# Kernel tuning notes

Measured on AMD Instinct MI355X. Metric: run time of the kernel, lower is better.

Reference implementation:

```python
import jax, jax.numpy as jnp
import numpy as np

# 8 directional difference stencils (N, S, E, W, NE, SE, SW, NW), OIHW [8,1,3,3]
_WINDOWS = np.array([
    [[0, 1, 0], [0, -1, 0], [0, 0, 0]],
    [[0, 0, 0], [0, -1, 0], [0, 1, 0]],
    [[0, 0, 0], [0, -1, 1], [0, 0, 0]],
    [[0, 0, 0], [1, -1, 0], [0, 0, 0]],
    [[0, 0, 1], [0, -1, 0], [0, 0, 0]],
    [[0, 0, 0], [0, -1, 0], [0, 0, 1]],
    [[0, 0, 0], [0, -1, 0], [1, 0, 0]],
    [[1, 0, 0], [0, -1, 0], [0, 0, 0]],
], dtype=np.float32).reshape(8, 1, 3, 3)

ITERATIONS = 30  # int(self.iterations.item()) with init value 30.0


def setup_inputs() -> dict:
    key = jax.random.key(0)
    k1, k2, k3 = jax.random.split(key, 3)
    x = jax.random.normal(k1, (32, 3, 512, 512), dtype=jnp.float32)
    W_expand = jax.random.normal(k2, (3, 3, 1, 1), dtype=jnp.float32) * 0.3
    b_expand = jax.random.normal(k3, (3,), dtype=jnp.float32) * 0.1
    return {
        "x": x,
        "delta": jnp.float32(0.1),
        "kappa": jnp.float32(15.0),
        "W_expand": W_expand,
        "b_expand": b_expand,
    }


def reference(x, delta, kappa, W_expand, b_expand):
    K = jnp.asarray(_WINDOWS)  # [8,1,3,3]
    # axial directions weight 1, diagonal directions weight 1/(sqrt(2))^2 = 0.5
    dir_w = jnp.array([1.0, 1.0, 1.0, 1.0, 0.5, 0.5, 0.5, 0.5],
                      dtype=x.dtype).reshape(1, 8, 1, 1)

    # RGB -> luminance, [B,1,H,W]
    u = (0.299 * x[:, 0] + 0.587 * x[:, 1] + 0.114 * x[:, 2])[:, None]

    def step(u, _):
        # all 8 directional gradients in one grouped conv: [B,8,H,W]
        nabla = jax.lax.conv_general_dilated(
            u, K, window_strides=(1, 1), padding='SAME',
            dimension_numbers=('NCHW', 'OIHW', 'NCHW'))
        diff = 1.0 / (1.0 + (nabla / kappa) ** 2)  # Perona-Malik diffusivity
        upd = jnp.sum(dir_w * diff * nabla, axis=1, keepdims=True)
        return u + delta * upd, None

    u, _ = jax.lax.scan(step, u, None, length=ITERATIONS)

    # repeat to 3 channels then 1x1 conv (expand_channels)
    u_rgb = jnp.repeat(u, 3, axis=1)  # [B,3,H,W]
    out = jnp.einsum('oi,bihw->bohw', W_expand[:, :, 0, 0], u_rgb)
    out = out + b_expand[None, :, None, None]
    return out
```

## Files before the change

kernel.cpp:

```cpp
#include <hip/hip_runtime.h>

#define BATCH 32
#define HGT 512
#define WID 512
#define PLANE (HGT * WID)
#define NPIX (BATCH * PLANE)
#define BSTRIDE (3 * PLANE)
#define WQ (WID / 4)
#define NQUAD (NPIX / 4)

#define RSLAB 16
#define SLABS (HGT / RSLAB)
#define LROWS (RSLAB + 4)
#define BROWS (RSLAB + 2)
#define FBLOCKS (BATCH * SLABS)
#define FTHREADS 512
#define LDS_BYTES ((LROWS + BROWS) * WID * 4)

__device__ __forceinline__ float4 ld4(const float* p) {
    return *reinterpret_cast<const float4*>(p);
}
__device__ __forceinline__ void st4(float* p, float4 v) {
    *reinterpret_cast<float4*>(p) = v;
}

__device__ __forceinline__ float pm_flux(float d, float ik2) {
    return d * __builtin_amdgcn_rcpf(fmaf(d * d, ik2, 1.f));
}

__device__ __forceinline__ void lds_row6(const float* __restrict__ buf, int row, int quad,
                                         float r[6]) {
    const float* p = buf + row * WID + (quad << 2);
    float4 v = ld4(p);
    r[1] = v.x; r[2] = v.y; r[3] = v.z; r[4] = v.w;
    r[0] = (quad > 0) ? p[-1] : 0.f;
    r[5] = (quad < WQ - 1) ? p[4] : 0.f;
}

__device__ __forceinline__ void level_flux(const float a[6], const float b[6],
                                           float vF[4], float seF[5], float swF[5],
                                           float ik2) {
#pragma unroll
    for (int j = 0; j < 4; ++j) vF[j] = pm_flux(b[j + 1] - a[j + 1], ik2);
#pragma unroll
    for (int i = 0; i < 5; ++i) seF[i] = pm_flux(b[i + 1] - a[i], ik2);
#pragma unroll
    for (int i = 0; i < 5; ++i) swF[i] = pm_flux(b[i] - a[i + 1], ik2);
}

template <typename Emit>
__device__ __forceinline__ void strip_from_lds(const float* __restrict__ buf, int L0, int n,
                                               int quad, float delta, float ik2,
                                               Emit&& emit) {
    float a[6], m[6], d6[6];
    lds_row6(buf, L0 - 1, quad, a);
    lds_row6(buf, L0, quad, m);
    float pV[4], pSE[5], pSW[5];
    level_flux(a, m, pV, pSE, pSW, ik2);

    for (int i = 0; i < n; ++i) {
        lds_row6(buf, L0 + i + 1, quad, d6);
        float hF[5];
#pragma unroll
        for (int t = 0; t < 5; ++t) hF[t] = pm_flux(m[t + 1] - m[t], ik2);
        float cV[4], cSE[5], cSW[5];
        level_flux(m, d6, cV, cSE, cSW, ik2);
        float o[4];
#pragma unroll
        for (int j = 0; j < 4; ++j) {
            float axial = cV[j] - pV[j] + hF[j + 1] - hF[j];
            float diag  = cSE[j + 1] + cSW[j] - pSE[j] - pSW[j + 1];
            o[j] = fmaf(delta, fmaf(0.5f, diag, axial), m[j + 1]);
        }
        emit(L0 + i, make_float4(o[0], o[1], o[2], o[3]));
#pragma unroll
        for (int t = 0; t < 6; ++t) m[t] = d6[t];
#pragma unroll
        for (int j = 0; j < 4; ++j) pV[j] = cV[j];
#pragma unroll
        for (int t = 0; t < 5; ++t) { pSE[t] = cSE[t]; pSW[t] = cSW[t]; }
    }
}

template <int MODE>
__global__ __launch_bounds__(FTHREADS, 4)
void pm_fused2(const float* __restrict__ src, int sstr,
               float* __restrict__ dst, int dstr,
               const float* __restrict__ pdelta, const float* __restrict__ pkappa,
               const float* __restrict__ Wexp, const float* __restrict__ bexp) {
    extern __shared__ float lds[];
    float* bufA = lds;
    float* bufB = lds + LROWS * WID;

    const int img  = blockIdx.x >> 5;
    const int slab = blockIdx.x & (SLABS - 1);
    const int H0   = slab * RSLAB;
    const int tid  = threadIdx.x;

    const float delta = *pdelta;
    const float kappa = *pkappa;
    const float ik2 = __builtin_amdgcn_rcpf(kappa * kappa);

    const float* sb = src + (size_t)img * sstr;
#pragma unroll
    for (int i = tid; i < LROWS * WQ; i += FTHREADS) {
        int row  = i >> 7;
        int quad = i & (WQ - 1);
        int g = H0 - 2 + row;
        float4 v = make_float4(0.f, 0.f, 0.f, 0.f);
        if ((unsigned)g < (unsigned)HGT) {
            const float* p = sb + g * WID + (quad << 2);
            if (MODE == 0) {
                float4 r = ld4(p), gg = ld4(p + PLANE), bb = ld4(p + 2 * PLANE);
                v.x = fmaf(0.299f, r.x, fmaf(0.587f, gg.x, 0.114f * bb.x));
                v.y = fmaf(0.299f, r.y, fmaf(0.587f, gg.y, 0.114f * bb.y));
                v.z = fmaf(0.299f, r.z, fmaf(0.587f, gg.z, 0.114f * bb.z));
                v.w = fmaf(0.299f, r.w, fmaf(0.587f, gg.w, 0.114f * bb.w));
            } else {
                v = ld4(p);
            }
        }
        st4(bufA + row * WID + (quad << 2), v);
    }
    __syncthreads();

    const int strip = tid >> 7;
    const int quad  = tid & (WQ - 1);

    {
        int L0 = 1 + 5 * strip - (strip == 3 ? 1 : 0);
        int n  = (strip < 2) ? 5 : 4;
        strip_from_lds(bufA, L0, n, quad, delta, ik2, [&](int L, float4 o) {
            int g = H0 - 2 + L;
            if ((unsigned)g >= (unsigned)HGT) o = make_float4(0.f, 0.f, 0.f, 0.f);
            st4(bufB + (L - 1) * WID + (quad << 2), o);
        });
    }
    __syncthreads();

    float s0 = 0.f, s1 = 0.f, s2 = 0.f, b0 = 0.f, b1 = 0.f, b2 = 0.f;
    if (MODE == 2) {
        s0 = Wexp[0] + Wexp[1] + Wexp[2];
        s1 = Wexp[3] + Wexp[4] + Wexp[5];
        s2 = Wexp[6] + Wexp[7] + Wexp[8];
        b0 = bexp[0]; b1 = bexp[1]; b2 = bexp[2];
    }
    {
        int LB0 = 1 + 4 * strip;
        float* db = dst + (size_t)img * dstr;
        strip_from_lds(bufB, LB0, 4, quad, delta, ik2, [&](int LB, float4 o) {
            int g = H0 - 1 + LB;
            float* p = db + g * WID + (quad << 2);
            if (MODE == 2) {
                st4(p, make_float4(fmaf(s0, o.x, b0), fmaf(s0, o.y, b0),
                                   fmaf(s0, o.z, b0), fmaf(s0, o.w, b0)));
                st4(p + PLANE, make_float4(fmaf(s1, o.x, b1), fmaf(s1, o.y, b1),
                                           fmaf(s1, o.z, b1), fmaf(s1, o.w, b1)));
                st4(p + 2 * PLANE, make_float4(fmaf(s2, o.x, b2), fmaf(s2, o.y, b2),
                                               fmaf(s2, o.z, b2), fmaf(s2, o.w, b2)));
            } else {
                st4(p, o);
            }
        });
    }
}

__global__ void expand_own_v4(float* __restrict__ out,
                              const float* __restrict__ Wexp,
                              const float* __restrict__ bexp) {
    int idx = blockIdx.x * blockDim.x + threadIdx.x;
    if (idx >= NQUAD) return;
    int b = idx / (PLANE / 4);
    int off = (idx - b * (PLANE / 4)) * 4;
    size_t base = (size_t)b * BSTRIDE + off;

    float4 u = ld4(out + base);
    float s0 = Wexp[0] + Wexp[1] + Wexp[2];
    float s1 = Wexp[3] + Wexp[4] + Wexp[5];
    float s2 = Wexp[6] + Wexp[7] + Wexp[8];
    float b0 = bexp[0], b1 = bexp[1], b2 = bexp[2];

    st4(out + base, make_float4(s0 * u.x + b0, s0 * u.y + b0, s0 * u.z + b0, s0 * u.w + b0));
    st4(out + base + PLANE,
        make_float4(s1 * u.x + b1, s1 * u.y + b1, s1 * u.z + b1, s1 * u.w + b1));
    st4(out + base + 2 * PLANE,
        make_float4(s2 * u.x + b2, s2 * u.y + b2, s2 * u.z + b2, s2 * u.w + b2));
}

extern "C" void kernel_launch(void* const* d_in, const int* in_sizes, int n_in,
                              void* d_out, int out_size, void* d_ws, size_t ws_size,
                              hipStream_t stream) {
    const float* x      = (const float*)d_in[0];
    const float* pdelta = (const float*)d_in[1];
    const float* pkappa = (const float*)d_in[2];
    const float* Wexp   = (const float*)d_in[3];
    const float* bexp   = (const float*)d_in[4];
    float* out = (float*)d_out;

    const size_t need = (size_t)2 * NPIX * sizeof(float);
    if (ws_size >= need) {
        float* uA = (float*)d_ws;
        float* uB = uA + NPIX;
        pm_fused2<0><<<FBLOCKS, FTHREADS, LDS_BYTES, stream>>>(
            x, BSTRIDE, uA, PLANE, pdelta, pkappa, Wexp, bexp);
        float* s = uA;
        float* d = uB;
        for (int k = 0; k < 13; ++k) {
            pm_fused2<1><<<FBLOCKS, FTHREADS, LDS_BYTES, stream>>>(
                s, PLANE, d, PLANE, pdelta, pkappa, Wexp, bexp);
            float* t = s; s = d; d = t;
        }
        pm_fused2<2><<<FBLOCKS, FTHREADS, LDS_BYTES, stream>>>(
            s, PLANE, out, BSTRIDE, pdelta, pkappa, Wexp, bexp);
    } else {
        float* uA = out;
        float* uB = out + PLANE;
        pm_fused2<0><<<FBLOCKS, FTHREADS, LDS_BYTES, stream>>>(
            x, BSTRIDE, uA, BSTRIDE, pdelta, pkappa, Wexp, bexp);
        float* s = uA;
        float* d = uB;
        for (int k = 0; k < 14; ++k) {
            pm_fused2<1><<<FBLOCKS, FTHREADS, LDS_BYTES, stream>>>(
                s, BSTRIDE, d, BSTRIDE, pdelta, pkappa, Wexp, bexp);
            float* t = s; s = d; d = t;
        }
        const int block = 256;
        const int grid_q = (NQUAD + block - 1) / block;
        expand_own_v4<<<grid_q, block, 0, stream>>>(out, Wexp, bexp);
    }
}
```

Baseline: 388.7 us.

## Generalize temporal blocking to S fused diffusion steps per launch with single LDS buffer

Templates the fused kernel on the number of time steps S done in LDS per launch, using one in-place buffer with register staging and barriers in place of two ping-pong buffers. The default path now runs 7 launches of 4 steps plus one launch of 2, where it previously ran 15 launches of 2 steps. This cuts global memory round-trips and launch count. In exchange, each launch recomputes wider halos (8 extra rows per 16-row slab), uses more LDS, and adds barriers between steps.

```diff
diff --git a/kernel.cpp b/kernel.cpp
--- a/kernel.cpp
+++ b/kernel.cpp
@@ -11,11 +11,8 @@
 
 #define RSLAB 16
 #define SLABS (HGT / RSLAB)
-#define LROWS (RSLAB + 4)
-#define BROWS (RSLAB + 2)
 #define FBLOCKS (BATCH * SLABS)
-#define FTHREADS 512
-#define LDS_BYTES ((LROWS + BROWS) * WID * 4)
+#define FT 512
 
 __device__ __forceinline__ float4 ld4(const float* p) {
     return *reinterpret_cast<const float4*>(p);
@@ -48,54 +45,28 @@
     for (int i = 0; i < 5; ++i) swF[i] = pm_flux(b[i] - a[i + 1], ik2);
 }
 
-template <typename Emit>
-__device__ __forceinline__ void strip_from_lds(const float* __restrict__ buf, int L0, int n,
-                                               int quad, float delta, float ik2,
-                                               Emit&& emit) {
-    float a[6], m[6], d6[6];
-    lds_row6(buf, L0 - 1, quad, a);
-    lds_row6(buf, L0, quad, m);
-    float pV[4], pSE[5], pSW[5];
-    level_flux(a, m, pV, pSE, pSW, ik2);
-
-    for (int i = 0; i < n; ++i) {
-        lds_row6(buf, L0 + i + 1, quad, d6);
-        float hF[5];
-#pragma unroll
-        for (int t = 0; t < 5; ++t) hF[t] = pm_flux(m[t + 1] - m[t], ik2);
-        float cV[4], cSE[5], cSW[5];
-        level_flux(m, d6, cV, cSE, cSW, ik2);
-        float o[4];
-#pragma unroll
-        for (int j = 0; j < 4; ++j) {
-            float axial = cV[j] - pV[j] + hF[j + 1] - hF[j];
-            float diag  = cSE[j + 1] + cSW[j] - pSE[j] - pSW[j + 1];
-            o[j] = fmaf(delta, fmaf(0.5f, diag, axial), m[j + 1]);
-        }
-        emit(L0 + i, make_float4(o[0], o[1], o[2], o[3]));
-#pragma unroll
-        for (int t = 0; t < 6; ++t) m[t] = d6[t];
-#pragma unroll
-        for (int j = 0; j < 4; ++j) pV[j] = cV[j];
-#pragma unroll
-        for (int t = 0; t < 5; ++t) { pSE[t] = cSE[t]; pSW[t] = cSW[t]; }
-    }
-}
-
-template <int MODE>
-__global__ __launch_bounds__(FTHREADS, 4)
-void pm_fused2(const float* __restrict__ src, int sstr,
+__device__ __forceinline__ void srange(int L0, int L1, int strip, int& s0, int& n) {
+    int tot = L1 - L0;
+    int base = tot >> 2, rem = tot & 3;
+    n = base + (strip < rem ? 1 : 0);
+    s0 = L0 + strip * base + (strip < rem ? strip : rem);
+}
+
+template <int MODE, int S>
+__global__ __launch_bounds__(FT, 4)
+void pm_fusedk(const float* __restrict__ src, int sstr,
                float* __restrict__ dst, int dstr,
                const float* __restrict__ pdelta, const float* __restrict__ pkappa,
                const float* __restrict__ Wexp, const float* __restrict__ bexp) {
-    extern __shared__ float lds[];
-    float* bufA = lds;
-    float* bufB = lds + LROWS * WID;
-
-    const int img  = blockIdx.x >> 5;
-    const int slab = blockIdx.x & (SLABS - 1);
-    const int H0   = slab * RSLAB;
-    const int tid  = threadIdx.x;
+    constexpr int LR = RSLAB + 2 * S;
+    extern __shared__ float buf[];
+
+    const int img   = blockIdx.x >> 5;
+    const int slab  = blockIdx.x & (SLABS - 1);
+    const int H0    = slab * RSLAB;
+    const int tid   = threadIdx.x;
+    const int strip = tid >> 7;
+    const int quad  = tid & (WQ - 1);
 
     const float delta = *pdelta;
     const float kappa = *pkappa;
@@ -103,13 +74,13 @@
 
     const float* sb = src + (size_t)img * sstr;
 #pragma unroll
-    for (int i = tid; i < LROWS * WQ; i += FTHREADS) {
-        int row  = i >> 7;
-        int quad = i & (WQ - 1);
-        int g = H0 - 2 + row;
+    for (int i = tid; i < LR * WQ; i += FT) {
+        int row = i >> 7;
+        int q   = i & (WQ - 1);
+        int g = H0 - S + row;
         float4 v = make_float4(0.f, 0.f, 0.f, 0.f);
         if ((unsigned)g < (unsigned)HGT) {
-            const float* p = sb + g * WID + (quad << 2);
+            const float* p = sb + g * WID + (q << 2);
             if (MODE == 0) {
                 float4 r = ld4(p), gg = ld4(p + PLANE), bb = ld4(p + 2 * PLANE);
                 v.x = fmaf(0.299f, r.x, fmaf(0.587f, gg.x, 0.114f * bb.x));
@@ -120,71 +91,115 @@
                 v = ld4(p);
             }
         }
-        st4(bufA + row * WID + (quad << 2), v);
+        st4(buf + row * WID + (q << 2), v);
     }
     __syncthreads();
 
-    const int strip = tid >> 7;
-    const int quad  = tid & (WQ - 1);
-
-    {
-        int L0 = 1 + 5 * strip - (strip == 3 ? 1 : 0);
-        int n  = (strip < 2) ? 5 : 4;
-        strip_from_lds(bufA, L0, n, quad, delta, ik2, [&](int L, float4 o) {
-            int g = H0 - 2 + L;
-            if ((unsigned)g >= (unsigned)HGT) o = make_float4(0.f, 0.f, 0.f, 0.f);
-            st4(bufB + (L - 1) * WID + (quad << 2), o);
-        });
-    }
-    __syncthreads();
-
-    float s0 = 0.f, s1 = 0.f, s2 = 0.f, b0 = 0.f, b1 = 0.f, b2 = 0.f;
+    float s0c = 0.f, s1c = 0.f, s2c = 0.f, b0c = 0.f, b1c = 0.f, b2c = 0.f;
     if (MODE == 2) {
-        s0 = Wexp[0] + Wexp[1] + Wexp[2];
-        s1 = Wexp[3] + Wexp[4] + Wexp[5];
-        s2 = Wexp[6] + Wexp[7] + Wexp[8];
-        b0 = bexp[0]; b1 = bexp[1]; b2 = bexp[2];
-    }
-    {
-        int LB0 = 1 + 4 * strip;
-        float* db = dst + (size_t)img * dstr;
-        strip_from_lds(bufB, LB0, 4, quad, delta, ik2, [&](int LB, float4 o) {
-            int g = H0 - 1 + LB;
-            float* p = db + g * WID + (quad << 2);
-            if (MODE == 2) {
-                st4(p, make_float4(fmaf(s0, o.x, b0), fmaf(s0, o.y, b0),
-                                   fmaf(s0, o.z, b0), fmaf(s0, o.w, b0)));
-                st4(p + PLANE, make_float4(fmaf(s1, o.x, b1), fmaf(s1, o.y, b1),
-                                           fmaf(s1, o.z, b1), fmaf(s1, o.w, b1)));
-                st4(p + 2 * PLANE, make_float4(fmaf(s2, o.x, b2), fmaf(s2, o.y, b2),
-                                               fmaf(s2, o.z, b2), fmaf(s2, o.w, b2)));
-            } else {
-                st4(p, o);
+        s0c = Wexp[0] + Wexp[1] + Wexp[2];
+        s1c = Wexp[3] + Wexp[4] + Wexp[5];
+        s2c = Wexp[6] + Wexp[7] + Wexp[8];
+        b0c = bexp[0]; b1c = bexp[1]; b2c = bexp[2];
+    }
+
+    float* db = dst + (size_t)img * dstr;
+
+#pragma unroll
+    for (int s = 0; s < S; ++s) {
+        const int L0r = s + 1, L1r = LR - 1 - s;
+        int st0, n;
+        srange(L0r, L1r, strip, st0, n);
+
+        float4 res[6];
+        float a[6], m[6], d6[6];
+        lds_row6(buf, st0 - 1, quad, a);
+        lds_row6(buf, st0, quad, m);
+        float pV[4], pSE[5], pSW[5];
+        level_flux(a, m, pV, pSE, pSW, ik2);
+
+#pragma unroll
+        for (int i = 0; i < 6; ++i) {
+            if (i < n) {
+                lds_row6(buf, st0 + i + 1, quad, d6);
+                float hF[5];
+#pragma unroll
+                for (int t = 0; t < 5; ++t) hF[t] = pm_flux(m[t + 1] - m[t], ik2);
+                float cV[4], cSE[5], cSW[5];
+                level_flux(m, d6, cV, cSE, cSW, ik2);
+                float o[4];
+#pragma unroll
+                for (int j = 0; j < 4; ++j) {
+                    float axial = cV[j] - pV[j] + hF[j + 1] - hF[j];
+                    float diag  = cSE[j + 1] + cSW[j] - pSE[j] - pSW[j + 1];
+                    o[j] = fmaf(delta, fmaf(0.5f, diag, axial), m[j + 1]);
+                }
+                int g = H0 - S + st0 + i;
+                bool in = (unsigned)g < (unsigned)HGT;
+                res[i] = in ? make_float4(o[0], o[1], o[2], o[3])
+                            : make_float4(0.f, 0.f, 0.f, 0.f);
+#pragma unroll
+                for (int t = 0; t < 6; ++t) m[t] = d6[t];
+#pragma unroll
+                for (int j = 0; j < 4; ++j) pV[j] = cV[j];
+#pragma unroll
+                for (int t = 0; t < 5; ++t) { pSE[t] = cSE[t]; pSW[t] = cSW[t]; }
             }
-        });
-    }
-}
-
-__global__ void expand_own_v4(float* __restrict__ out,
-                              const float* __restrict__ Wexp,
-                              const float* __restrict__ bexp) {
+        }
+
+        if (s == S - 1) {
+#pragma unroll
+            for (int i = 0; i < 6; ++i) {
+                if (i < n) {
+                    int g = H0 - S + st0 + i;
+                    float* p = db + g * WID + (quad << 2);
+                    if (MODE == 2) {
+                        float4 u = res[i];
+                        st4(p, make_float4(fmaf(s0c, u.x, b0c), fmaf(s0c, u.y, b0c),
+                                           fmaf(s0c, u.z, b0c), fmaf(s0c, u.w, b0c)));
+                        st4(p + PLANE,
+                            make_float4(fmaf(s1c, u.x, b1c), fmaf(s1c, u.y, b1c),
+                                        fmaf(s1c, u.z, b1c), fmaf(s1c, u.w, b1c)));
+                        st4(p + 2 * PLANE,
+                            make_float4(fmaf(s2c, u.x, b2c), fmaf(s2c, u.y, b2c),
+                                        fmaf(s2c, u.z, b2c), fmaf(s2c, u.w, b2c)));
+                    } else {
+                        st4(p, res[i]);
+                    }
+                }
+            }
+        } else {
+            __syncthreads();
+#pragma unroll
+            for (int i = 0; i < 6; ++i)
+                if (i < n) st4(buf + (st0 + i) * WID + (quad << 2), res[i]);
+            __syncthreads();
+        }
+    }
+}
+
+__global__ void expand_from(const float* __restrict__ usrc, int ustr,
+                            float* __restrict__ out,
+                            const float* __restrict__ Wexp,
+                            const float* __restrict__ bexp) {
     int idx = blockIdx.x * blockDim.x + threadIdx.x;
     if (idx >= NQUAD) return;
     int b = idx / (PLANE / 4);
     int off = (idx - b * (PLANE / 4)) * 4;
-    size_t base = (size_t)b * BSTRIDE + off;
-
-    float4 u = ld4(out + base);
+
+    float4 u = ld4(usrc + (size_t)b * ustr + off);
     float s0 = Wexp[0] + Wexp[1] + Wexp[2];
     float s1 = Wexp[3] + Wexp[4] + Wexp[5];
     float s2 = Wexp[6] + Wexp[7] + Wexp[8];
     float b0 = bexp[0], b1 = bexp[1], b2 = bexp[2];
 
-    st4(out + base, make_float4(s0 * u.x + b0, s0 * u.y + b0, s0 * u.z + b0, s0 * u.w + b0));
-    st4(out + base + PLANE,
-        make_float4(s1 * u.x + b1, s1 * u.y + b1, s1 * u.z + b1, s1 * u.w + b1));
-    st4(out + base + 2 * PLANE,
-        make_float4(s2 * u.x + b2, s2 * u.y + b2, s2 * u.z + b2, s2 * u.w + b2));
+    size_t base = (size_t)b * BSTRIDE + off;
+    st4(out + base, make_float4(fmaf(s0, u.x, b0), fmaf(s0, u.y, b0),
+                                fmaf(s0, u.z, b0), fmaf(s0, u.w, b0)));
+    st4(out + base + PLANE, make_float4(fmaf(s1, u.x, b1), fmaf(s1, u.y, b1),
+                                        fmaf(s1, u.z, b1), fmaf(s1, u.w, b1)));
+    st4(out + base + 2 * PLANE, make_float4(fmaf(s2, u.x, b2), fmaf(s2, u.y, b2),
+                                            fmaf(s2, u.z, b2), fmaf(s2, u.w, b2)));
 }
 
 extern "C" void kernel_launch(void* const* d_in, const int* in_sizes, int n_in,
@@ -197,35 +212,40 @@
     const float* bexp   = (const float*)d_in[4];
     float* out = (float*)d_out;
 
+    const int LDS4 = (RSLAB + 8) * WID * 4;
+    const int LDS2 = (RSLAB + 4) * WID * 4;
+
     const size_t need = (size_t)2 * NPIX * sizeof(float);
     if (ws_size >= need) {
         float* uA = (float*)d_ws;
         float* uB = uA + NPIX;
-        pm_fused2<0><<<FBLOCKS, FTHREADS, LDS_BYTES, stream>>>(
+        pm_fusedk<0, 4><<<FBLOCKS, FT, LDS4, stream>>>(
             x, BSTRIDE, uA, PLANE, pdelta, pkappa, Wexp, bexp);
         float* s = uA;
         float* d = uB;
-        for (int k = 0; k < 13; ++k) {
-            pm_fused2<1><<<FBLOCKS, FTHREADS, LDS_BYTES, stream>>>(
+        for (int k = 0; k < 6; ++k) {
+            pm_fusedk<1, 4><<<FBLOCKS, FT, LDS4, stream>>>(
                 s, PLANE, d, PLANE, pdelta, pkappa, Wexp, bexp);
             float* t = s; s = d; d = t;
         }
-        pm_fused2<2><<<FBLOCKS, FTHREADS, LDS_BYTES, stream>>>(
+        pm_fusedk<2, 2><<<FBLOCKS, FT, LDS2, stream>>>(
             s, PLANE, out, BSTRIDE, pdelta, pkappa, Wexp, bexp);
     } else {
         float* uA = out;
         float* uB = out + PLANE;
-        pm_fused2<0><<<FBLOCKS, FTHREADS, LDS_BYTES, stream>>>(
+        pm_fusedk<0, 4><<<FBLOCKS, FT, LDS4, stream>>>(
             x, BSTRIDE, uA, BSTRIDE, pdelta, pkappa, Wexp, bexp);
         float* s = uA;
         float* d = uB;
-        for (int k = 0; k < 14; ++k) {
-            pm_fused2<1><<<FBLOCKS, FTHREADS, LDS_BYTES, stream>>>(
+        for (int k = 0; k < 6; ++k) {
+            pm_fusedk<1, 4><<<FBLOCKS, FT, LDS4, stream>>>(
                 s, BSTRIDE, d, BSTRIDE, pdelta, pkappa, Wexp, bexp);
             float* t = s; s = d; d = t;
         }
+        pm_fusedk<1, 2><<<FBLOCKS, FT, LDS2, stream>>>(
+            s, BSTRIDE, d, BSTRIDE, pdelta, pkappa, Wexp, bexp);
         const int block = 256;
         const int grid_q = (NQUAD + block - 1) / block;
-        expand_own_v4<<<grid_q, block, 0, stream>>>(out, Wexp, bexp);
-    }
-}
+        expand_from<<<grid_q, block, 0, stream>>>(d, BSTRIDE, out, Wexp, bexp);
+    }
+}
```

Result: faster. 375.9 us (-3.3%).
